# Optimization experiments

Hardware: AMD Instinct MI355X
Metric: run time of the kernel (lower is better)

The kernel has to match this reference:

```python
import jax, jax.numpy as jnp
import numpy as np

BLOCK_SIZE = 64
N_EMBD = 128
N_HEAD = 4
HEAD_DIM = N_EMBD // N_HEAD  # 32


def setup_inputs() -> dict:
    key = jax.random.key(0)
    kx, kq, kk, kv = jax.random.split(key, 4)
    B, T = 4096, 64
    x = jax.random.normal(kx, (B, T, N_EMBD), dtype=jnp.float32)
    # nn.Linear(n_embd, head_dim, bias=False): stored as [out,in] in torch,
    # here kept as [in, out] = [128, 32] so projection is x @ W.
    s = 1.0 / np.sqrt(N_EMBD)
    Wq = jax.random.uniform(kq, (N_EMBD, HEAD_DIM), jnp.float32, -s, s)
    Wk = jax.random.uniform(kk, (N_EMBD, HEAD_DIM), jnp.float32, -s, s)
    Wv = jax.random.uniform(kv, (N_EMBD, HEAD_DIM), jnp.float32, -s, s)
    return {"x": x, "Wq": Wq, "Wk": Wk, "Wv": Wv}


def reference(x, Wq, Wk, Wv):
    B, T, C = x.shape
    q = x @ Wq  # [B, T, Hd]
    k = x @ Wk
    v = x @ Wv
    scale = 1.0 / jnp.sqrt(jnp.asarray(k.shape[-1], x.dtype))
    wei = jnp.einsum("btd,bsd->bts", q, k) * scale  # [B, T, T]
    causal = jnp.tril(jnp.ones((T, T), dtype=bool))
    wei = jnp.where(causal, wei, -jnp.inf)
    wei = jax.nn.softmax(wei, axis=-1)
    out = jnp.einsum("bts,bsd->btd", wei, v)  # [B, T, Hd]
    return out
```

## Files before the change

kernel.cpp:

```cpp
#include <hip/hip_runtime.h>


#define TT 64
#define CC 128
#define HD 32

typedef __bf16 bf16_t;
typedef __bf16 bf8_t __attribute__((ext_vector_type(8)));
typedef __bf16 bf4_t __attribute__((ext_vector_type(4)));
typedef float  f4_t  __attribute__((ext_vector_type(4)));

__global__ __launch_bounds__(256) void head_fused(
    const float* __restrict__ x, const float* __restrict__ Wq,
    const float* __restrict__ Wk, const float* __restrict__ Wv,
    float* __restrict__ out)
{
  __shared__ __align__(16) bf16_t xs[TT][136];
  __shared__ __align__(16) bf16_t wt[96][136];
  __shared__ __align__(16) bf16_t qs[TT][40];
  __shared__ __align__(16) bf16_t ks[TT][40];
  __shared__ __align__(16) bf16_t vt[HD][72];

  const int tid  = threadIdx.x;
  const int wave = tid >> 6;
  const int lane = tid & 63;
  const int quad = lane >> 4;
  const int l16  = lane & 15;
  const int b    = blockIdx.x;

  const float4* x4 = (const float4*)(x + (size_t)b * (TT * CC));
  #pragma unroll
  for (int i = 0; i < 8; ++i) {
    int e = tid + i * 256;
    float4 f = x4[e];
    int fi = e << 2;
    int row = fi >> 7, col = fi & 127;
    bf4_t h = { (bf16_t)f.x, (bf16_t)f.y, (bf16_t)f.z, (bf16_t)f.w };
    *(bf4_t*)&xs[row][col] = h;
  }
  {
    const float* Ws[3] = { Wq, Wk, Wv };
    #pragma unroll
    for (int m = 0; m < 3; ++m) {
      const float* W = Ws[m];
      #pragma unroll
      for (int i = 0; i < 16; ++i) {
        int e = tid + i * 256;
        float wv_ = W[e];
        int k = e >> 5, n = e & 31;
        wt[m * 32 + n][k] = (bf16_t)wv_;
      }
    }
  }
  __syncthreads();

  f4_t zero4 = {0.f, 0.f, 0.f, 0.f};
  f4_t acc[6];
  #pragma unroll
  for (int n = 0; n < 6; ++n) acc[n] = zero4;
  #pragma unroll
  for (int kk = 0; kk < 4; ++kk) {
    int k0 = kk * 32 + quad * 8;
    bf8_t a = *(const bf8_t*)&xs[wave * 16 + l16][k0];
    #pragma unroll
    for (int n = 0; n < 6; ++n) {
      bf8_t bb = *(const bf8_t*)&wt[n * 16 + l16][k0];
      acc[n] = __builtin_amdgcn_mfma_f32_16x16x32_bf16(a, bb, acc[n], 0, 0, 0);
    }
  }
  #pragma unroll
  for (int r = 0; r < 4; ++r) {
    int row = wave * 16 + quad * 4 + r;
    qs[row][l16]      = (bf16_t)acc[0][r];
    qs[row][16 + l16] = (bf16_t)acc[1][r];
    ks[row][l16]      = (bf16_t)acc[2][r];
    ks[row][16 + l16] = (bf16_t)acc[3][r];
    vt[l16][row]      = (bf16_t)acc[4][r];
    vt[16 + l16][row] = (bf16_t)acc[5][r];
  }
  __syncthreads();

  bf16_t (*ps)[72] = (bf16_t(*)[72])&xs[0][0];
  f4_t sc[4];
  #pragma unroll
  for (int nt = 0; nt < 4; ++nt) sc[nt] = zero4;
  {
    bf8_t aq = *(const bf8_t*)&qs[wave * 16 + l16][quad * 8];
    #pragma unroll
    for (int nt = 0; nt < 4; ++nt) {
      if (nt <= wave) {
        bf8_t bk = *(const bf8_t*)&ks[nt * 16 + l16][quad * 8];
        sc[nt] = __builtin_amdgcn_mfma_f32_16x16x32_bf16(aq, bk, zero4, 0, 0, 0);
      }
    }
  }
  const float scale = 0.17677669529663687f;
  #pragma unroll
  for (int r = 0; r < 4; ++r) {
    int rl = quad * 4 + r;
    float vals[4];
    float vmax = -INFINITY;
    #pragma unroll
    for (int nt = 0; nt < 4; ++nt) {
      float v_ = -INFINITY;
      if (nt < wave)                         v_ = sc[nt][r] * scale;
      else if (nt == wave && l16 <= rl)      v_ = sc[nt][r] * scale;
      vals[nt] = v_;
      vmax = fmaxf(vmax, v_);
    }
    #pragma unroll
    for (int off = 1; off < 16; off <<= 1)
      vmax = fmaxf(vmax, __shfl_xor(vmax, off));
    float psum = 0.f;
    #pragma unroll
    for (int nt = 0; nt < 4; ++nt) {
      float p = (vals[nt] == -INFINITY) ? 0.f : __expf(vals[nt] - vmax);
      vals[nt] = p;
      psum += p;
    }
    #pragma unroll
    for (int off = 1; off < 16; off <<= 1)
      psum += __shfl_xor(psum, off);
    float inv = 1.0f / psum;
    int row = wave * 16 + rl;
    #pragma unroll
    for (int nt = 0; nt < 4; ++nt)
      ps[row][nt * 16 + l16] = (bf16_t)(vals[nt] * inv);
  }
  __syncthreads();

  f4_t o0 = zero4, o1 = zero4;
  #pragma unroll
  for (int kk = 0; kk < 2; ++kk) {
    int k0 = kk * 32 + quad * 8;
    bf8_t ap  = *(const bf8_t*)&ps[wave * 16 + l16][k0];
    bf8_t bv0 = *(const bf8_t*)&vt[l16][k0];
    bf8_t bv1 = *(const bf8_t*)&vt[16 + l16][k0];
    o0 = __builtin_amdgcn_mfma_f32_16x16x32_bf16(ap, bv0, o0, 0, 0, 0);
    o1 = __builtin_amdgcn_mfma_f32_16x16x32_bf16(ap, bv1, o1, 0, 0, 0);
  }
  float* ob = out + (size_t)b * (TT * HD);
  #pragma unroll
  for (int r = 0; r < 4; ++r) {
    int row = wave * 16 + quad * 4 + r;
    ob[row * HD + l16]      = o0[r];
    ob[row * HD + 16 + l16] = o1[r];
  }
}

extern "C" void kernel_launch(void* const* d_in, const int* in_sizes, int n_in,
                              void* d_out, int out_size, void* d_ws, size_t ws_size,
                              hipStream_t stream) {
  const float* x  = (const float*)d_in[0];
  const float* Wq = (const float*)d_in[1];
  const float* Wk = (const float*)d_in[2];
  const float* Wv = (const float*)d_in[3];
  float* out = (float*)d_out;
  int B = in_sizes[0] / (TT * CC);
  head_fused<<<dim3(B), dim3(256), 0, stream>>>(x, Wq, Wk, Wv, out);
}
```

Measured before the change: 227.0 us.

## Pre-pack bf16 weights in MFMA fragment layout via separate prep kernel

Result: faster. 219.0 us (-3.5%).

```diff
diff --git a/kernel.cpp b/kernel.cpp
--- a/kernel.cpp
+++ b/kernel.cpp
@@ -10,13 +10,26 @@
 typedef __bf16 bf4_t __attribute__((ext_vector_type(4)));
 typedef float  f4_t  __attribute__((ext_vector_type(4)));
 
+__global__ __launch_bounds__(256) void prep_weights(
+    const float* __restrict__ Wq, const float* __restrict__ Wk,
+    const float* __restrict__ Wv, bf16_t* __restrict__ wf)
+{
+  int t = blockIdx.x * 256 + threadIdx.x;
+  int j    = t & 7;
+  int lane = (t >> 3) & 63;
+  int kt   = (t >> 9) & 3;
+  int n6   = t >> 11;
+  int k    = kt * 32 + (lane >> 4) * 8 + j;
+  int col  = (n6 & 1) * 16 + (lane & 15);
+  const float* W = (n6 >> 1) == 0 ? Wq : ((n6 >> 1) == 1 ? Wk : Wv);
+  wf[t] = (bf16_t)W[k * HD + col];
+}
+
 __global__ __launch_bounds__(256) void head_fused(
-    const float* __restrict__ x, const float* __restrict__ Wq,
-    const float* __restrict__ Wk, const float* __restrict__ Wv,
+    const float* __restrict__ x, const bf8_t* __restrict__ wf,
     float* __restrict__ out)
 {
   __shared__ __align__(16) bf16_t xs[TT][136];
-  __shared__ __align__(16) bf16_t wt[96][136];
   __shared__ __align__(16) bf16_t qs[TT][40];
   __shared__ __align__(16) bf16_t ks[TT][40];
   __shared__ __align__(16) bf16_t vt[HD][72];
@@ -38,20 +51,6 @@
     bf4_t h = { (bf16_t)f.x, (bf16_t)f.y, (bf16_t)f.z, (bf16_t)f.w };
     *(bf4_t*)&xs[row][col] = h;
   }
-  {
-    const float* Ws[3] = { Wq, Wk, Wv };
-    #pragma unroll
-    for (int m = 0; m < 3; ++m) {
-      const float* W = Ws[m];
-      #pragma unroll
-      for (int i = 0; i < 16; ++i) {
-        int e = tid + i * 256;
-        float wv_ = W[e];
-        int k = e >> 5, n = e & 31;
-        wt[m * 32 + n][k] = (bf16_t)wv_;
-      }
-    }
-  }
   __syncthreads();
 
   f4_t zero4 = {0.f, 0.f, 0.f, 0.f};
@@ -64,7 +63,7 @@
     bf8_t a = *(const bf8_t*)&xs[wave * 16 + l16][k0];
     #pragma unroll
     for (int n = 0; n < 6; ++n) {
-      bf8_t bb = *(const bf8_t*)&wt[n * 16 + l16][k0];
+      bf8_t bb = wf[(n * 4 + kk) * 64 + lane];
       acc[n] = __builtin_amdgcn_mfma_f32_16x16x32_bf16(a, bb, acc[n], 0, 0, 0);
     }
   }
@@ -156,6 +155,9 @@
   const float* Wk = (const float*)d_in[2];
   const float* Wv = (const float*)d_in[3];
   float* out = (float*)d_out;
+  bf16_t* wf = (bf16_t*)d_ws;
   int B = in_sizes[0] / (TT * CC);
-  head_fused<<<dim3(B), dim3(256), 0, stream>>>(x, Wq, Wk, Wv, out);
+
+  prep_weights<<<dim3(48), dim3(256), 0, stream>>>(Wq, Wk, Wv, wf);
+  head_fused<<<dim3(B), dim3(256), 0, stream>>>(x, (const bf8_t*)wf, out);
 }
```
